# Kernel tuning notes

Measured on AMD Instinct MI355X. Metric: run time of the kernel, lower is better.

The kernel has to match this reference:

```python
import jax, jax.numpy as jnp
import numpy as np

NUM_HEADS = 12
LN_EPS = 1e-5


def _layernorm(t, w, b):
    # LayerNorm over last dim (head_dim), biased variance as in torch
    mu = jnp.mean(t, axis=-1, keepdims=True)
    var = jnp.mean(jnp.square(t - mu), axis=-1, keepdims=True)
    return (t - mu) * jax.lax.rsqrt(var + LN_EPS) * w + b


def _apply_rope(t, cos, sin):
    # t: [B, H, S, D]; cos/sin: [S, D//2]; interleaved complex pairs (torch view_as_complex)
    tr = t[..., 0::2]
    ti = t[..., 1::2]
    c = cos[None, None, :, :]
    s = sin[None, None, :, :]
    out_r = tr * c - ti * s
    out_i = tr * s + ti * c
    return jnp.stack([out_r, out_i], axis=-1).reshape(t.shape)


def setup_inputs() -> dict:
    key = jax.random.key(0)
    ks = jax.random.split(key, 6)
    B, N, C = 16, 1024, 768
    H = NUM_HEADS
    D = C // H  # 64
    P, L = 1, 32
    rot_len = N - P - L  # 991
    x = jax.random.normal(ks[0], (B, N, C), dtype=jnp.float32)
    # rotary frequencies (llama-style)
    inv_freq = 1.0 / (10000.0 ** (np.arange(0, D, 2, dtype=np.float32) / D))
    angles = np.arange(rot_len, dtype=np.float32)[:, None] * inv_freq[None, :]
    cos = jnp.asarray(np.cos(angles))
    sin = jnp.asarray(np.sin(angles))
    # parameters (qkv_bias=False, qk_norm=True)
    w_qkv = jax.random.normal(ks[1], (C, 3 * C), dtype=jnp.float32) * (C ** -0.5)
    q_ln_w = jnp.ones((D,), jnp.float32)
    q_ln_b = jnp.zeros((D,), jnp.float32)
    k_ln_w = jnp.ones((D,), jnp.float32)
    k_ln_b = jnp.zeros((D,), jnp.float32)
    w_proj = jax.random.normal(ks[2], (C, C), dtype=jnp.float32) * (C ** -0.5)
    b_proj = jnp.zeros((C,), jnp.float32)
    return {
        "x": x, "cos": cos, "sin": sin,
        "w_qkv": w_qkv,
        "q_ln_w": q_ln_w, "q_ln_b": q_ln_b,
        "k_ln_w": k_ln_w, "k_ln_b": k_ln_b,
        "w_proj": w_proj, "b_proj": b_proj,
        "num_prefix_tokens": 1, "num_latent_tokens": 32,
    }


def reference(x, cos, sin, w_qkv, q_ln_w, q_ln_b, k_ln_w, k_ln_b, w_proj, b_proj,
              num_prefix_tokens, num_latent_tokens):
    B, N, C = x.shape
    H = NUM_HEADS
    D = C // H
    P, L = num_prefix_tokens, num_latent_tokens
    scale = D ** -0.5

    qkv = (x @ w_qkv).reshape(B, N, 3, H, D)
    qkv = jnp.transpose(qkv, (2, 0, 3, 1, 4))  # [3, B, H, N, D]
    q, k, v = qkv[0], qkv[1], qkv[2]

    q = _layernorm(q, q_ln_w, q_ln_b)
    k = _layernorm(k, k_ln_w, k_ln_b)

    # partial RoPE: only the middle [P : N-L] tokens are rotated
    q_rot = _apply_rope(q[:, :, P:N - L], cos, sin)
    k_rot = _apply_rope(k[:, :, P:N - L], cos, sin)
    q = jnp.concatenate([q[:, :, :P], q_rot, q[:, :, N - L:]], axis=2)
    k = jnp.concatenate([k[:, :, :P], k_rot, k[:, :, N - L:]], axis=2)

    attn = jnp.einsum("bhqd,bhkd->bhqk", q * scale, k)
    attn = jax.nn.softmax(attn, axis=-1)
    out = jnp.einsum("bhqk,bhkd->bhqd", attn, v)
    out = jnp.transpose(out, (0, 2, 1, 3)).reshape(B, N, C)
    return out @ w_proj + b_proj
```

## Files before the change

### kernel.cpp

```cpp
#include <hip/hip_runtime.h>
#include <hip/hip_bf16.h>

typedef __attribute__((ext_vector_type(8))) short v8s;
typedef __attribute__((ext_vector_type(4))) short v4s;
typedef __attribute__((ext_vector_type(4))) float f32x4;

__device__ __forceinline__ float bf2f(short s){
  unsigned u = ((unsigned)(unsigned short)s) << 16;
  float f; __builtin_memcpy(&f, &u, 4); return f;
}
__device__ __forceinline__ short f2bf(float f){
  unsigned u; __builtin_memcpy(&u, &f, 4);
  unsigned r = (u + 0x7FFFu + ((u >> 16) & 1u)) >> 16;
  return (short)r;
}

__device__ __forceinline__ void gload16(const void* g, void* l){
  __builtin_amdgcn_global_load_lds((const __attribute__((address_space(1))) void*)g,
                                   (__attribute__((address_space(3))) void*)l, 16, 0, 0);
}

__global__ __launch_bounds__(256) void k_cast8(const float* __restrict__ in,
                                               short* __restrict__ out, long n){
  long i = ((long)blockIdx.x * 256 + threadIdx.x) * 8;
  long stride = (long)gridDim.x * 256 * 8;
  for (; i < n; i += stride){
    float4 a = *(const float4*)(in + i);
    float4 b = *(const float4*)(in + i + 4);
    v8s v;
    v[0]=f2bf(a.x); v[1]=f2bf(a.y); v[2]=f2bf(a.z); v[3]=f2bf(a.w);
    v[4]=f2bf(b.x); v[5]=f2bf(b.y); v[6]=f2bf(b.z); v[7]=f2bf(b.w);
    *(v8s*)(out + i) = v;
  }
}

__global__ __launch_bounds__(256) void k_tcast(const float* __restrict__ in,
                                               short* __restrict__ out, int R, int Cc){
  __shared__ float T[32][33];
  int tx = threadIdx.x & 31, ty = threadIdx.x >> 5;
  int r0 = blockIdx.x * 32, c0 = blockIdx.y * 32;
  #pragma unroll
  for (int p = 0; p < 4; p++){
    int r = ty + p*8;
    T[r][tx] = in[(long)(r0 + r)*Cc + c0 + tx];
  }
  __syncthreads();
  #pragma unroll
  for (int p = 0; p < 4; p++){
    int r = ty + p*8;
    out[(long)(c0 + r)*R + r0 + tx] = f2bf(T[tx][r]);
  }
}

template<int OUT_MODE>
__global__ __launch_bounds__(256) void k_gemm(const short* __restrict__ A,
                                              const short* __restrict__ Bt,
                                              void* __restrict__ Cout,
                                              const float* __restrict__ bias,
                                              int M, int N, int K){
  __shared__ short As[128*64];
  __shared__ short Bs[128*64];
  int row0 = blockIdx.x * 128, col0 = blockIdx.y * 128;
  int t = threadIdx.x;
  int lane = t & 63, w = t >> 6;
  int g = lane >> 4, r16 = lane & 15;
  int wr = w >> 1, wc = w & 1;
  int rsw = (r16 & 7) << 3;
  int srow = t >> 3;
  int scol = ((t & 7) * 8) ^ ((srow & 7) << 3);
  f32x4 acc[4][4];
  #pragma unroll
  for (int mi = 0; mi < 4; mi++)
    #pragma unroll
    for (int ni = 0; ni < 4; ni++)
      acc[mi][ni] = (f32x4){0.f,0.f,0.f,0.f};

  for (int kt = 0; kt < K; kt += 64){
    #pragma unroll
    for (int p = 0; p < 4; p++){
      int rr = p*32 + srow;
      gload16(&A[(long)(row0 + rr)*K + kt + scol], &As[(p*256 + w*64)*8]);
    }
    #pragma unroll
    for (int p = 0; p < 4; p++){
      int rr = p*32 + srow;
      gload16(&Bt[(long)(col0 + rr)*K + kt + scol], &Bs[(p*256 + w*64)*8]);
    }
    __syncthreads();
    #pragma unroll
    for (int ks = 0; ks < 2; ks++){
      v8s af[4], bfr[4];
      #pragma unroll
      for (int mi = 0; mi < 4; mi++)
        af[mi] = *(const v8s*)&As[(wr*64 + mi*16 + r16)*64 + ((ks*32 + g*8) ^ rsw)];
      #pragma unroll
      for (int ni = 0; ni < 4; ni++)
        bfr[ni] = *(const v8s*)&Bs[(wc*64 + ni*16 + r16)*64 + ((ks*32 + g*8) ^ rsw)];
      #pragma unroll
      for (int mi = 0; mi < 4; mi++)
        #pragma unroll
        for (int ni = 0; ni < 4; ni++)
          acc[mi][ni] = __builtin_amdgcn_mfma_f32_16x16x32_bf16(af[mi], bfr[ni], acc[mi][ni], 0, 0, 0);
    }
    __syncthreads();
  }
  #pragma unroll
  for (int mi = 0; mi < 4; mi++)
    #pragma unroll
    for (int ni = 0; ni < 4; ni++){
      int rbase = row0 + wr*64 + mi*16 + g*4;
      int cc = col0 + wc*64 + ni*16 + r16;
      #pragma unroll
      for (int j = 0; j < 4; j++){
        float v = acc[mi][ni][j];
        if (OUT_MODE == 0)
          ((short*)Cout)[(long)(rbase + j)*N + cc] = f2bf(v);
        else
          ((float*)Cout)[(long)(rbase + j)*N + cc] = v + bias[cc];
      }
    }
}

__global__ __launch_bounds__(256) void k_lnrope(const short* __restrict__ QKV,
     const float* __restrict__ cosT, const float* __restrict__ sinT,
     const float* __restrict__ qw, const float* __restrict__ qb,
     const float* __restrict__ kw, const float* __restrict__ kb,
     short* __restrict__ Qb, short* __restrict__ Kb, short* __restrict__ Vt){
  __shared__ short Vs[64][72];
  int blk = blockIdx.x;
  int ntile = blk & 15, h = (blk >> 4) % 12, b = blk / 192;
  int t = threadIdx.x;
  int tl = t >> 2, ch = t & 3;
  int n = ntile*64 + tl;
  long row = (long)(b*1024 + n) * 2304;
  int d0 = ch * 16;
  long outrow = ((long)(b*12 + h)*1024 + n) * 64;

  #pragma unroll
  for (int sel = 0; sel < 2; sel++){
    const short* src = &QKV[row + sel*768 + h*64 + d0];
    float f[16];
    v8s a0 = *(const v8s*)src;
    v8s a1 = *(const v8s*)(src + 8);
    #pragma unroll
    for (int i = 0; i < 8; i++){ f[i] = bf2f(a0[i]); f[8+i] = bf2f(a1[i]); }
    float s1 = 0.f, s2 = 0.f;
    #pragma unroll
    for (int i = 0; i < 16; i++){ s1 += f[i]; s2 += f[i]*f[i]; }
    s1 += __shfl_xor(s1, 1); s2 += __shfl_xor(s2, 1);
    s1 += __shfl_xor(s1, 2); s2 += __shfl_xor(s2, 2);
    float mu = s1 * (1.0f/64.0f);
    float var = s2 * (1.0f/64.0f) - mu*mu;
    float rs = rsqrtf(var + 1e-5f);
    const float* wp = sel ? kw : qw;
    const float* bp = sel ? kb : qb;
    #pragma unroll
    for (int i = 0; i < 16; i++) f[i] = (f[i] - mu)*rs*wp[d0+i] + bp[d0+i];
    if (n >= 1 && n < 992){
      int pos = n - 1;
      const float* cp = &cosT[pos*32 + ch*8];
      const float* sp = &sinT[pos*32 + ch*8];
      #pragma unroll
      for (int i = 0; i < 8; i++){
        float c = cp[i], s = sp[i];
        float tr = f[2*i], ti = f[2*i+1];
        f[2*i]   = tr*c - ti*s;
        f[2*i+1] = tr*s + ti*c;
      }
    }
    if (sel == 0){
      #pragma unroll
      for (int i = 0; i < 16; i++) f[i] *= 0.18033688011112042f;
    }
    v8s o0, o1;
    #pragma unroll
    for (int i = 0; i < 8; i++){ o0[i] = f2bf(f[i]); o1[i] = f2bf(f[8+i]); }
    short* dst = sel ? &Kb[outrow + d0] : &Qb[outrow + d0];
    *(v8s*)dst = o0;
    *(v8s*)(dst + 8) = o1;
  }
  {
    const short* vsrc = &QKV[row + 1536 + h*64 + d0];
    *(v8s*)&Vs[tl][d0]     = *(const v8s*)vsrc;
    *(v8s*)&Vs[tl][d0 + 8] = *(const v8s*)(vsrc + 8);
  }
  __syncthreads();
  {
    int d = tl, nch = ch;
    v8s o0, o1;
    #pragma unroll
    for (int i = 0; i < 8; i++){ o0[i] = Vs[nch*16 + i][d]; o1[i] = Vs[nch*16 + 8 + i][d]; }
    long vrow = ((long)(b*12 + h)*64 + d)*1024 + ntile*64 + nch*16;
    *(v8s*)&Vt[vrow]     = o0;
    *(v8s*)&Vt[vrow + 8] = o1;
  }
}

__global__ __launch_bounds__(512) void k_attn(const short* __restrict__ Qb,
                                              const short* __restrict__ Kb,
                                              const short* __restrict__ Vt,
                                              short* __restrict__ O){
  __shared__ short Ks[64*64];
  __shared__ short Vts[64*64];
  int blk = blockIdx.x;
  int qt = blk & 7, h = (blk >> 3) % 12, b = blk / 96;
  long bh = b*12 + h;
  int t = threadIdx.x, lane = t & 63, w = t >> 6;
  int g = lane >> 4, r16 = lane & 15;
  int rsw = (r16 & 7) << 3;
  int q0 = qt*128 + w*16;

  int srow = t >> 3;
  int scol = ((t & 7) * 8) ^ ((srow & 7) << 3);
  const short* Ksrc = &Kb[(bh*1024 + srow)*64 + scol];
  const short* Vsrc = &Vt[(bh*64 + srow)*1024 + scol];
  short* KsBase  = &Ks[w*512];
  short* VtsBase = &Vts[w*512];

  v8s bq[2];
  #pragma unroll
  for (int tt = 0; tt < 2; tt++)
    bq[tt] = *(const v8s*)&Qb[(bh*1024 + q0 + r16)*64 + tt*32 + g*8];

  f32x4 oacc[4];
  #pragma unroll
  for (int t2 = 0; t2 < 4; t2++) oacc[t2] = (f32x4){0.f,0.f,0.f,0.f};
  float m_run = -1e30f, l_run = 0.f;

  for (int kt = 0; kt < 1024; kt += 64){
    gload16(Ksrc + kt*64, KsBase);
    gload16(Vsrc + kt,    VtsBase);
    __syncthreads();

    f32x4 sacc[4];
    #pragma unroll
    for (int f = 0; f < 4; f++) sacc[f] = (f32x4){0.f,0.f,0.f,0.f};
    #pragma unroll
    for (int tt = 0; tt < 2; tt++){
      #pragma unroll
      for (int f = 0; f < 4; f++){
        v8s ak = *(const v8s*)&Ks[(f*16 + r16)*64 + ((tt*32 + g*8) ^ rsw)];
        sacc[f] = __builtin_amdgcn_mfma_f32_16x16x32_bf16(ak, bq[tt], sacc[f], 0, 0, 0);
      }
    }
    float mt = -1e30f;
    #pragma unroll
    for (int f = 0; f < 4; f++)
      #pragma unroll
      for (int j = 0; j < 4; j++) mt = fmaxf(mt, sacc[f][j]);
    mt = fmaxf(mt, __shfl_xor(mt, 16));
    mt = fmaxf(mt, __shfl_xor(mt, 32));
    float m_new = fmaxf(m_run, mt);
    float alpha = exp2f(m_run - m_new);
    float p[4][4];
    float lsum = 0.f;
    #pragma unroll
    for (int f = 0; f < 4; f++)
      #pragma unroll
      for (int j = 0; j < 4; j++){
        p[f][j] = exp2f(sacc[f][j] - m_new);
        lsum += p[f][j];
      }
    lsum += __shfl_xor(lsum, 16);
    lsum += __shfl_xor(lsum, 32);
    l_run = l_run*alpha + lsum;
    m_run = m_new;
    float aj4[4];
    #pragma unroll
    for (int j = 0; j < 4; j++) aj4[j] = __shfl(alpha, 4*g + j, 64);
    #pragma unroll
    for (int t2 = 0; t2 < 4; t2++)
      #pragma unroll
      for (int j = 0; j < 4; j++) oacc[t2][j] *= aj4[j];

    v8s pa[4];
    #pragma unroll
    for (int f = 0; f < 4; f++){
      #pragma unroll
      for (int j = 0; j < 4; j++) pa[f][j] = f2bf(p[f][j]);
      #pragma unroll
      for (int j = 4; j < 8; j++) pa[f][j] = 0;
    }
    #pragma unroll
    for (int t2 = 0; t2 < 4; t2++)
      #pragma unroll
      for (int f = 0; f < 4; f++){
        v4s v4 = *(const v4s*)&Vts[(t2*16 + r16)*64 + ((f*16 + g*4) ^ rsw)];
        v8s bv;
        bv[0]=v4[0]; bv[1]=v4[1]; bv[2]=v4[2]; bv[3]=v4[3];
        bv[4]=0; bv[5]=0; bv[6]=0; bv[7]=0;
        oacc[t2] = __builtin_amdgcn_mfma_f32_16x16x32_bf16(pa[f], bv, oacc[t2], 0, 0, 0);
      }
    __syncthreads();
  }
  float linv = 1.0f / l_run;
  float lj[4];
  #pragma unroll
  for (int j = 0; j < 4; j++) lj[j] = __shfl(linv, 4*g + j, 64);
  #pragma unroll
  for (int t2 = 0; t2 < 4; t2++)
    #pragma unroll
    for (int j = 0; j < 4; j++){
      float v = oacc[t2][j] * lj[j];
      O[((long)b*1024 + q0 + 4*g + j)*768 + h*64 + t2*16 + r16] = f2bf(v);
    }
}

extern "C" void kernel_launch(void* const* d_in, const int* in_sizes, int n_in,
                              void* d_out, int out_size, void* d_ws, size_t ws_size,
                              hipStream_t stream) {
  const float* x      = (const float*)d_in[0];
  const float* cosT   = (const float*)d_in[1];
  const float* sinT   = (const float*)d_in[2];
  const float* w_qkv  = (const float*)d_in[3];
  const float* q_ln_w = (const float*)d_in[4];
  const float* q_ln_b = (const float*)d_in[5];
  const float* k_ln_w = (const float*)d_in[6];
  const float* k_ln_b = (const float*)d_in[7];
  const float* w_proj = (const float*)d_in[8];
  const float* b_proj = (const float*)d_in[9];

  char* ws = (char*)d_ws;
  short* Xb       = (short*)(ws);
  short* Wqkv_bt  = (short*)(ws + 25165824);
  short* Wproj_bt = (short*)(ws + 28704768);
  short* QKV      = (short*)(ws + 29884416);
  short* Qb       = (short*)(ws + 105381888);
  short* Kb       = (short*)(ws + 130547712);
  short* Vt       = (short*)(ws + 155713536);
  short* O        = (short*)(ws + 180879360);

  k_cast8<<<6144, 256, 0, stream>>>(x, Xb, 12582912L);
  k_tcast<<<dim3(24, 72), 256, 0, stream>>>(w_qkv, Wqkv_bt, 768, 2304);
  k_tcast<<<dim3(24, 24), 256, 0, stream>>>(w_proj, Wproj_bt, 768, 768);
  k_gemm<0><<<dim3(128, 18), 256, 0, stream>>>(Xb, Wqkv_bt, QKV, nullptr, 16384, 2304, 768);
  k_lnrope<<<3072, 256, 0, stream>>>(QKV, cosT, sinT, q_ln_w, q_ln_b, k_ln_w, k_ln_b, Qb, Kb, Vt);
  k_attn<<<1536, 512, 0, stream>>>(Qb, Kb, Vt, O);
  k_gemm<1><<<dim3(128, 6), 256, 0, stream>>>(O, Wproj_bt, d_out, b_proj, 16384, 768, 768);
}
```

Measured before the change: 393.0 us.

## Pack P into full-K MFMA operands, use cvt_pk_bf16, and raise MFMA priority

The PV product previously zero-padded half of each 16x16x32 MFMA operand, so 16 MFMAs did the work of 8. It now packs two 16-key P fragments into one full operand, pairs them with matching V halves, and issues 8 MFMAs per tile. The P-to-bf16 conversion uses the packed v_cvt_pk_bf16_f32 instruction instead of software rounding. s_setprio brackets around MFMA groups in the GEMM and attention loops aim to favour matrix issue across waves. This relies on the lane-to-k mapping of the packed operands matching the V half-loads exactly, and any mismatch would give wrong results.

```diff
diff --git a/kernel.cpp b/kernel.cpp
--- a/kernel.cpp
+++ b/kernel.cpp
@@ -13,6 +13,11 @@
   unsigned u; __builtin_memcpy(&u, &f, 4);
   unsigned r = (u + 0x7FFFu + ((u >> 16) & 1u)) >> 16;
   return (short)r;
+}
+__device__ __forceinline__ unsigned cvtpk(float a, float b){
+  unsigned r;
+  asm("v_cvt_pk_bf16_f32 %0, %1, %2" : "=v"(r) : "v"(a), "v"(b));
+  return r;
 }
 
 __device__ __forceinline__ void gload16(const void* g, void* l){
@@ -96,11 +101,13 @@
       #pragma unroll
       for (int ni = 0; ni < 4; ni++)
         bfr[ni] = *(const v8s*)&Bs[(wc*64 + ni*16 + r16)*64 + ((ks*32 + g*8) ^ rsw)];
+      __builtin_amdgcn_s_setprio(1);
       #pragma unroll
       for (int mi = 0; mi < 4; mi++)
         #pragma unroll
         for (int ni = 0; ni < 4; ni++)
           acc[mi][ni] = __builtin_amdgcn_mfma_f32_16x16x32_bf16(af[mi], bfr[ni], acc[mi][ni], 0, 0, 0);
+      __builtin_amdgcn_s_setprio(0);
     }
     __syncthreads();
   }
@@ -237,11 +244,15 @@
     for (int f = 0; f < 4; f++) sacc[f] = (f32x4){0.f,0.f,0.f,0.f};
     #pragma unroll
     for (int tt = 0; tt < 2; tt++){
-      #pragma unroll
-      for (int f = 0; f < 4; f++){
-        v8s ak = *(const v8s*)&Ks[(f*16 + r16)*64 + ((tt*32 + g*8) ^ rsw)];
-        sacc[f] = __builtin_amdgcn_mfma_f32_16x16x32_bf16(ak, bq[tt], sacc[f], 0, 0, 0);
-      }
+      v8s ak[4];
+      #pragma unroll
+      for (int f = 0; f < 4; f++)
+        ak[f] = *(const v8s*)&Ks[(f*16 + r16)*64 + ((tt*32 + g*8) ^ rsw)];
+      __builtin_amdgcn_s_setprio(1);
+      #pragma unroll
+      for (int f = 0; f < 4; f++)
+        sacc[f] = __builtin_amdgcn_mfma_f32_16x16x32_bf16(ak[f], bq[tt], sacc[f], 0, 0, 0);
+      __builtin_amdgcn_s_setprio(0);
     }
     float mt = -1e30f;
     #pragma unroll
@@ -273,24 +284,28 @@
       #pragma unroll
       for (int j = 0; j < 4; j++) oacc[t2][j] *= aj4[j];
 
-    v8s pa[4];
-    #pragma unroll
-    for (int f = 0; f < 4; f++){
-      #pragma unroll
-      for (int j = 0; j < 4; j++) pa[f][j] = f2bf(p[f][j]);
-      #pragma unroll
-      for (int j = 4; j < 8; j++) pa[f][j] = 0;
-    }
-    #pragma unroll
-    for (int t2 = 0; t2 < 4; t2++)
-      #pragma unroll
-      for (int f = 0; f < 4; f++){
-        v4s v4 = *(const v4s*)&Vts[(t2*16 + r16)*64 + ((f*16 + g*4) ^ rsw)];
-        v8s bv;
-        bv[0]=v4[0]; bv[1]=v4[1]; bv[2]=v4[2]; bv[3]=v4[3];
-        bv[4]=0; bv[5]=0; bv[6]=0; bv[7]=0;
-        oacc[t2] = __builtin_amdgcn_mfma_f32_16x16x32_bf16(pa[f], bv, oacc[t2], 0, 0, 0);
+    unsigned d00 = cvtpk(p[0][0], p[0][1]), d01 = cvtpk(p[0][2], p[0][3]);
+    unsigned d10 = cvtpk(p[1][0], p[1][1]), d11 = cvtpk(p[1][2], p[1][3]);
+    unsigned d20 = cvtpk(p[2][0], p[2][1]), d21 = cvtpk(p[2][2], p[2][3]);
+    unsigned d30 = cvtpk(p[3][0], p[3][1]), d31 = cvtpk(p[3][2], p[3][3]);
+    union PU { v8s s; unsigned u[4]; };
+    PU pa0, pa1;
+    pa0.u[0]=d00; pa0.u[1]=d01; pa0.u[2]=d10; pa0.u[3]=d11;
+    pa1.u[0]=d20; pa1.u[1]=d21; pa1.u[2]=d30; pa1.u[3]=d31;
+
+    #pragma unroll
+    for (int t2 = 0; t2 < 4; t2++){
+      int vrow = (t2*16 + r16)*64;
+      #pragma unroll
+      for (int kb = 0; kb < 2; kb++){
+        union VU { v8s s; v4s h[2]; } vb;
+        vb.h[0] = *(const v4s*)&Vts[vrow + ((kb*32 + g*4) ^ rsw)];
+        vb.h[1] = *(const v4s*)&Vts[vrow + ((kb*32 + 16 + g*4) ^ rsw)];
+        __builtin_amdgcn_s_setprio(1);
+        oacc[t2] = __builtin_amdgcn_mfma_f32_16x16x32_bf16(kb ? pa1.s : pa0.s, vb.s, oacc[t2], 0, 0, 0);
+        __builtin_amdgcn_s_setprio(0);
       }
+    }
     __syncthreads();
   }
   float linv = 1.0f / l_run;
```

New measurement: 360.0 us. 1.09x faster.
